# Kernel optimization log

Measured on AMD Instinct MI355X. Metric: run time of the kernel, lower is better.

## Reference

```python
import jax, jax.numpy as jnp
import numpy as np

DAMPENING = 0.3          # dampening_factor
REC_DAMPENING = 0.4      # recurrent_dampening_factor
DT = 1.0
MAX_DELAY = 5
N_BASIS = 5


@jax.custom_vjp
def spike_function(v_scaled):
    # hard threshold with triangular pseudo-derivative (custom gradient)
    return (v_scaled > 0.0).astype(v_scaled.dtype)

def _spike_fwd(v_scaled):
    return spike_function(v_scaled), v_scaled

def _spike_bwd(v_scaled, g):
    return (g * DAMPENING * jnp.maximum(1.0 - jnp.abs(v_scaled), 0.0),)

spike_function.defvjp(_spike_fwd, _spike_bwd)


def setup_inputs() -> dict:
    key = jax.random.key(0)
    ks = jax.random.split(key, 12)
    N, E, T, B = 50000, 2_000_000, 40, 1
    D, n5 = MAX_DELAY, N * N_BASIS
    inp = {}
    inp['weights'] = jax.random.normal(ks[0], (E,), jnp.float32) * 0.01
    inp['edge_basis'] = jax.random.uniform(ks[1], (E, N_BASIS), jnp.float32)
    inp['ext_input'] = jax.random.normal(ks[2], (B, T, n5), jnp.float32) * 0.02
    inp['decay'] = 0.9 + 0.09 * jax.random.uniform(ks[3], (N,), jnp.float32)
    inp['current_factor'] = jax.random.uniform(ks[4], (N,), jnp.float32)
    inp['gathered_g'] = jax.random.normal(ks[5], (N,), jnp.float32) * 0.01
    inp['v_th'] = jnp.ones((N,), jnp.float32)          # normalized threshold
    inp['v_reset'] = jnp.zeros((N,), jnp.float32)
    inp['normalizer'] = jnp.ones((N,), jnp.float32)    # v_th - e_l
    inp['t_ref'] = 2.0 * jnp.ones((N,), jnp.float32)
    inp['exp_dt_k'] = 0.8 + 0.19 * jax.random.uniform(ks[6], (N, 2), jnp.float32)
    inp['asc_amps'] = jax.random.normal(ks[7], (N, 2), jnp.float32) * 0.01
    inp['syn_decay'] = jax.random.uniform(ks[8], (n5,), jnp.float32)
    inp['psc_initial'] = jax.random.uniform(ks[9], (n5,), jnp.float32)
    inp['pre_idx'] = jax.random.randint(ks[10], (E,), 0, D * N, jnp.int32)
    inp['post_idx'] = jax.random.randint(ks[11], (E,), 0, N, jnp.int32)
    return inp


def reference(weights, edge_basis, ext_input, decay, current_factor, gathered_g,
              v_th, v_reset, normalizer, t_ref, exp_dt_k, asc_amps,
              syn_decay, psc_initial, pre_idx, post_idx):
    B, T, n5 = ext_input.shape
    N = n5 // N_BASIS
    D = MAX_DELAY
    # per-edge weight across the 5 synaptic basis filters: [E,5]
    ew = weights[:, None] * edge_basis

    def rec_input(z_flat):  # z_flat: [B, D*N] delayed spike buffer (flattened)
        zg = jnp.take(z_flat, pre_idx, axis=1)                # [B,E] gather presynaptic spikes
        contrib = zg[:, :, None] * ew[None]                    # [B,E,5]
        out = jax.vmap(lambda c: jax.ops.segment_sum(c, post_idx, num_segments=N))(contrib)
        return out.reshape(B, N * N_BASIS)                     # [B,N*5]

    def step(carry, x_t):
        v, r, asc, psc, z_buf = carry
        # recurrent dampening: scale gradient through recurrent spikes
        zd = z_buf * REC_DAMPENING
        zb = jax.lax.stop_gradient(z_buf - zd) + zd
        i_rec = rec_input(zb.reshape(B, D * N))
        new_psc = psc * syn_decay + (i_rec + x_t) * psc_initial      # [B,N*5]
        input_current = new_psc.reshape(B, N, N_BASIS).sum(-1)       # [B,N]
        prev_z = z_buf[:, 0]                                         # most recent spikes
        new_asc = exp_dt_k * asc + prev_z[:, :, None] * asc_amps     # [B,N,2]
        c1 = input_current + new_asc.sum(-1) + gathered_g
        new_v = decay * v + current_factor * c1
        new_v = jnp.where(prev_z > 0.5, v_reset, new_v)              # hard reset
        v_sc = (new_v - v_th) / normalizer
        z = spike_function(v_sc)
        z = jnp.where(r > 0.0, jnp.zeros_like(z), z)                 # refractory block
        new_r = jnp.maximum(r + z * t_ref - DT, 0.0)
        new_buf = jnp.concatenate([z[:, None], z_buf[:, :-1]], axis=1)
        return (new_v, new_r, new_asc, new_psc, new_buf), z

    v0 = jnp.broadcast_to(v_reset, (B, N)).astype(jnp.float32)
    r0 = jnp.zeros((B, N), jnp.float32)
    asc0 = jnp.zeros((B, N, 2), jnp.float32)
    psc0 = jnp.zeros((B, n5), jnp.float32)
    buf0 = jnp.zeros((B, D, N), jnp.float32)
    x_seq = jnp.transpose(ext_input, (1, 0, 2))  # [T,B,N*5]
    _, z_seq = jax.lax.scan(step, (v0, r0, asc0, psc0, buf0), x_seq)
    return jnp.transpose(z_seq, (1, 0, 2))  # [B,T,N] spikes
```

## Files before the change

### kernel.cpp

```cpp
#include <hip/hip_runtime.h>

#define NB_ 5
#define MD_ 5
#define CSL 128
#define CAP 6144
#define CH2 4096
#define RING 6


__global__ __launch_bounds__(256) void partition_kernel(
    const int* __restrict__ pre_idx,
    int* __restrict__ gcur,
    unsigned* __restrict__ part,
    int E, int N)
{
    __shared__ unsigned srt[CH2];
    __shared__ unsigned short bkt[CH2];
    __shared__ int hist[512];
    __shared__ int lbase[512];
    __shared__ int pos[512];
    __shared__ int gbase[512];
    __shared__ int tmp[256];

    const int t  = threadIdx.x;
    const int e0 = blockIdx.x * CH2;
    const int cnt = min(CH2, E - e0);

    hist[t] = 0; hist[t + 256] = 0;
    __syncthreads();

    for (int i = t; i < cnt; i += 256) {
        int pre = pre_idx[e0 + i];
        int d = pre / N;
        int n = pre - d * N;
        atomicAdd(&hist[n >> 7], 1);
    }
    __syncthreads();

    int a = hist[2 * t], b = hist[2 * t + 1], s = a + b;
    tmp[t] = s;
    __syncthreads();
    int x = s;
    for (int off = 1; off < 256; off <<= 1) {
        int y = (t >= off) ? tmp[t - off] : 0;
        __syncthreads();
        x += y;
        tmp[t] = x;
        __syncthreads();
    }
    int ep = x - s;
    lbase[2 * t] = ep;         pos[2 * t] = ep;
    lbase[2 * t + 1] = ep + a; pos[2 * t + 1] = ep + a;
    gbase[2 * t]     = a ? atomicAdd(&gcur[2 * t], a) : 0;
    gbase[2 * t + 1] = b ? atomicAdd(&gcur[2 * t + 1], b) : 0;
    __syncthreads();

    for (int i = t; i < cnt; i += 256) {
        int pre = pre_idx[e0 + i];
        int d = pre / N;
        int n = pre - d * N;
        int bk = n >> 7;
        int p = atomicAdd(&pos[bk], 1);
        srt[p] = ((unsigned)(n & (CSL - 1)) << 24) | ((unsigned)d << 21)
               | (unsigned)(e0 + i);
        bkt[p] = (unsigned short)bk;
    }
    __syncthreads();

    for (int j = t; j < cnt; j += 256) {
        int bk = bkt[j];
        int off2 = gbase[bk] + (j - lbase[bk]);
        if (off2 < CAP)
            part[(size_t)bk * CAP + off2] = srt[j];
    }
}

__global__ __launch_bounds__(256) void bucket_sort_kernel(
    const int* __restrict__ gcur,
    const unsigned* __restrict__ part,
    unsigned* __restrict__ edgeRec,
    uint2* __restrict__ rp,
    const float* __restrict__ decay, const float* __restrict__ cf,
    const float* __restrict__ g,     const float* __restrict__ vth,
    const float* __restrict__ vrst,  const float* __restrict__ nrm,
    const float* __restrict__ tref,  const float* __restrict__ ek,
    const float* __restrict__ am,
    float4* __restrict__ pk, float* __restrict__ v,
    int N)
{
    __shared__ int h[CSL];
    __shared__ int sc_[CSL];
    __shared__ int pos_[CSL];
    int c = blockIdx.x, t = threadIdx.x;

    if (t < CSL) {
        int n = c * CSL + t;
        if (n < N) {
            pk[3 * n]     = make_float4(decay[n], cf[n], g[n], vth[n]);
            pk[3 * n + 1] = make_float4(vrst[n], nrm[n], tref[n], ek[2 * n]);
            pk[3 * n + 2] = make_float4(ek[2 * n + 1], am[2 * n], am[2 * n + 1], 0.0f);
            v[n] = vrst[n];
        }
    }

    int cnt = min(gcur[c], CAP);
    size_t base = (size_t)c * CAP;
    if (t < CSL) h[t] = 0;
    __syncthreads();
    for (int i = t; i < cnt; i += 256)
        atomicAdd(&h[part[base + i] >> 24], 1);
    __syncthreads();
    if (t < CSL) sc_[t] = h[t];
    __syncthreads();
    for (int off = 1; off < CSL; off <<= 1) {
        int y = 0;
        if (t < CSL && t >= off) y = sc_[t - off];
        __syncthreads();
        if (t < CSL && t >= off) sc_[t] += y;
        __syncthreads();
    }
    if (t < CSL) {
        int end = sc_[t];
        pos_[t] = (int)base + end - h[t];
        int gn = c * CSL + t;
        if (gn < N)
            rp[gn] = make_uint2((unsigned)(base + end - h[t]),
                                (unsigned)(base + end));
    }
    __syncthreads();
    for (int i = t; i < cnt; i += 256) {
        unsigned q = part[base + i];
        int dst = atomicAdd(&pos_[q >> 24], 1);
        edgeRec[dst] = q;
    }
}


__global__ __launch_bounds__(256) void step_kernel(
    const float* __restrict__ x_t,
    float*       __restrict__ psc,
    const float* __restrict__ sd,
    const float* __restrict__ pi,
    const float4* __restrict__ pk,
    float* __restrict__ v,
    float* __restrict__ r,
    float* __restrict__ asc,
    float* __restrict__ ring,
    const int* __restrict__ scnt,
    int*       __restrict__ scnt_new,
    const float* __restrict__ out_prev,
    float*       __restrict__ out_t,
    const uint2*    __restrict__ rp,
    const unsigned* __restrict__ edgeRec,
    const float*    __restrict__ weights,
    const float*    __restrict__ edge_basis,
    const int*      __restrict__ post_idx,
    int t, int n5, int N)
{
    const int tloc = threadIdx.x;
    const int n = blockIdx.x * blockDim.x + tloc;
    const bool has = (n < N);
    const int lane = tloc & 63;

    const int* sw = scnt + t;
    int scw = sw[0] + sw[1] + sw[2] + sw[3] + sw[4];

    float z = 0.0f;
    if (has) {
        float ir0 = 0.f, ir1 = 0.f, ir2 = 0.f, ir3 = 0.f, ir4 = 0.f;
        float* rg = ring + (size_t)(t % RING) * n5 + (size_t)n * NB_;
        if (scw > 0) {
            ir0 = rg[0]; ir1 = rg[1]; ir2 = rg[2]; ir3 = rg[3]; ir4 = rg[4];
            rg[0] = 0.f; rg[1] = 0.f; rg[2] = 0.f; rg[3] = 0.f; rg[4] = 0.f;
        }

        const float* xp  = x_t + (size_t)n * NB_;
        float*       pp  = psc + (size_t)n * NB_;
        const float* sdp = sd  + (size_t)n * NB_;
        const float* pip = pi  + (size_t)n * NB_;
        float ic = 0.0f, pv;
        pv = pp[0] * sdp[0] + (ir0 + xp[0]) * pip[0]; pp[0] = pv; ic += pv;
        pv = pp[1] * sdp[1] + (ir1 + xp[1]) * pip[1]; pp[1] = pv; ic += pv;
        pv = pp[2] * sdp[2] + (ir2 + xp[2]) * pip[2]; pp[2] = pv; ic += pv;
        pv = pp[3] * sdp[3] + (ir3 + xp[3]) * pip[3]; pp[3] = pv; ic += pv;
        pv = pp[4] * sdp[4] + (ir4 + xp[4]) * pip[4]; pp[4] = pv; ic += pv;

        float4 P0 = pk[3 * n], P1 = pk[3 * n + 1], P2 = pk[3 * n + 2];

        float pz = (t > 0) ? out_prev[n] : 0.0f;

        float a0 = P1.w * asc[2 * n]     + pz * P2.y;
        float a1 = P2.x * asc[2 * n + 1] + pz * P2.z;
        asc[2 * n]     = a0;
        asc[2 * n + 1] = a1;

        float c1 = ic + (a0 + a1) + P0.z;
        float nv = P0.x * v[n] + P0.y * c1;
        if (pz > 0.5f) nv = P1.x;

        float vsc = (nv - P0.w) / P1.y;
        z = (vsc > 0.0f) ? 1.0f : 0.0f;
        float rr = r[n];
        if (rr > 0.0f) z = 0.0f;

        r[n] = fmaxf(rr + z * P1.z - 1.0f, 0.0f);
        v[n] = nv;
        out_t[n] = z;
    }

    unsigned long long fm = __ballot(z != 0.0f);
    if (lane == 0 && fm)
        atomicAdd(scnt_new, (int)__popcll(fm));

    if (fm) {
        unsigned rs0 = 0, re0 = 0;
        if (z != 0.0f) { uint2 row = rp[n]; rs0 = row.x; re0 = row.y; }

        unsigned long long fm2 = fm;
        while (fm2) {
            int src = (int)(__ffsll((long long)fm2) - 1);
            fm2 &= fm2 - 1;
            unsigned rs = __shfl(rs0, src);
            unsigned re = __shfl(re0, src);
            for (unsigned i = rs + lane; i < re; i += 64) {
                unsigned q = edgeRec[i];
                int d = (int)((q >> 21) & 7u);
                int e = (int)(q & 0x1FFFFFu);
                float w = weights[e];
                const float* bs = edge_basis + (size_t)e * NB_;
                float* dst = ring + (size_t)((t + 1 + d) % RING) * n5
                           + (size_t)post_idx[e] * NB_;
                atomicAdd(dst + 0, w * bs[0]);
                atomicAdd(dst + 1, w * bs[1]);
                atomicAdd(dst + 2, w * bs[2]);
                atomicAdd(dst + 3, w * bs[3]);
                atomicAdd(dst + 4, w * bs[4]);
            }
        }
    }
}


extern "C" void kernel_launch(void* const* d_in, const int* in_sizes, int n_in,
                              void* d_out, int out_size, void* d_ws, size_t ws_size,
                              hipStream_t stream)
{
    const float* weights        = (const float*)d_in[0];
    const float* edge_basis     = (const float*)d_in[1];
    const float* ext_input      = (const float*)d_in[2];
    const float* decay          = (const float*)d_in[3];
    const float* current_factor = (const float*)d_in[4];
    const float* gathered_g     = (const float*)d_in[5];
    const float* v_th           = (const float*)d_in[6];
    const float* v_reset        = (const float*)d_in[7];
    const float* normalizer     = (const float*)d_in[8];
    const float* t_ref          = (const float*)d_in[9];
    const float* exp_dt_k       = (const float*)d_in[10];
    const float* asc_amps       = (const float*)d_in[11];
    const float* syn_decay      = (const float*)d_in[12];
    const float* psc_initial    = (const float*)d_in[13];
    const int*   pre_idx        = (const int*)d_in[14];
    const int*   post_idx       = (const int*)d_in[15];

    const int E  = in_sizes[0];
    const int N  = in_sizes[3];
    const int n5 = N * NB_;
    const int T  = in_sizes[2] / n5;

    const int NC = (N + CSL - 1) / CSL;

    float* out = (float*)d_out;

    char* wsb = (char*)d_ws;
    size_t o = 0;
    int*   gcur = (int*)(wsb + o);   o += 512 * 4;
    int*   scnt = (int*)(wsb + o);   o += (size_t)(T + MD_) * 4;
    o = (o + 15) & ~(size_t)15;
    float* psc  = (float*)(wsb + o); o += (size_t)n5 * 4;
    float* r    = (float*)(wsb + o); o += (size_t)N * 4;
    float* asc  = (float*)(wsb + o); o += (size_t)2 * N * 4;
    o = (o + 15) & ~(size_t)15;
    float* ring = (float*)(wsb + o); o += (size_t)RING * n5 * 4;
    size_t zero_bytes = o;
    float*  v       = (float*)(wsb + o);  o += (size_t)N * 4;
    float4* pk      = (float4*)(wsb + o); o += (size_t)N * 12 * 4;
    uint2*  rp      = (uint2*)(wsb + o);  o += (size_t)N * 8;
    o = (o + 15) & ~(size_t)15;
    unsigned* part    = (unsigned*)(wsb + o); o += (size_t)NC * CAP * 4;
    unsigned* edgeRec = (unsigned*)(wsb + o); o += (size_t)NC * CAP * 4;

    hipMemsetAsync(d_ws, 0, zero_bytes, stream);

    const int nbe = (E + CH2 - 1) / CH2;
    partition_kernel<<<nbe, 256, 0, stream>>>(pre_idx, gcur, part, E, N);
    bucket_sort_kernel<<<NC, 256, 0, stream>>>(
        gcur, part, edgeRec, rp,
        decay, current_factor, gathered_g, v_th, v_reset, normalizer, t_ref,
        exp_dt_k, asc_amps, pk, v, N);

    const int nblk = (N + 255) / 256;
    for (int t = 0; t < T; ++t) {
        step_kernel<<<nblk, 256, 0, stream>>>(
            ext_input + (size_t)t * n5,
            psc, syn_decay, psc_initial,
            pk, v, r, asc,
            ring, scnt, scnt + MD_ + t,
            out + (size_t)(t > 0 ? t - 1 : 0) * N,
            out + (size_t)t * N,
            rp, edgeRec, weights, edge_basis, post_idx,
            t, n5, N);
    }
}
```

Before: 251.5 us.

## Pack per-neuron constants and state into float4 AoS records for step kernel

Per-neuron constants (synaptic decay, psc initial, neuron params, CSR row range) go into six contiguous float4s, and mutable state (psc, asc, v, r, previous spike) into three float4s per neuron. Each step now does wide vector loads and stores instead of many scattered scalar accesses across separate arrays, and no longer re-reads the previous output. This cuts memory transactions per step. The cost is a larger per-neuron stride, with some unused padding lanes being loaded.

```diff
diff --git a/kernel.cpp b/kernel.cpp
--- a/kernel.cpp
+++ b/kernel.cpp
@@ -79,13 +79,13 @@
     const int* __restrict__ gcur,
     const unsigned* __restrict__ part,
     unsigned* __restrict__ edgeRec,
-    uint2* __restrict__ rp,
     const float* __restrict__ decay, const float* __restrict__ cf,
     const float* __restrict__ g,     const float* __restrict__ vth,
     const float* __restrict__ vrst,  const float* __restrict__ nrm,
     const float* __restrict__ tref,  const float* __restrict__ ek,
     const float* __restrict__ am,
-    float4* __restrict__ pk, float* __restrict__ v,
+    const float* __restrict__ sd,    const float* __restrict__ pi,
+    float4* __restrict__ constC, float4* __restrict__ state,
     int N)
 {
     __shared__ int h[CSL];
@@ -93,16 +93,6 @@
     __shared__ int pos_[CSL];
     int c = blockIdx.x, t = threadIdx.x;
 
-    if (t < CSL) {
-        int n = c * CSL + t;
-        if (n < N) {
-            pk[3 * n]     = make_float4(decay[n], cf[n], g[n], vth[n]);
-            pk[3 * n + 1] = make_float4(vrst[n], nrm[n], tref[n], ek[2 * n]);
-            pk[3 * n + 2] = make_float4(ek[2 * n + 1], am[2 * n], am[2 * n + 1], 0.0f);
-            v[n] = vrst[n];
-        }
-    }
-
     int cnt = min(gcur[c], CAP);
     size_t base = (size_t)c * CAP;
     if (t < CSL) h[t] = 0;
@@ -122,10 +112,24 @@
     if (t < CSL) {
         int end = sc_[t];
         pos_[t] = (int)base + end - h[t];
-        int gn = c * CSL + t;
-        if (gn < N)
-            rp[gn] = make_uint2((unsigned)(base + end - h[t]),
-                                (unsigned)(base + end));
+        int n = c * CSL + t;
+        if (n < N) {
+            unsigned rs = (unsigned)(base + end - h[t]);
+            unsigned re = (unsigned)(base + end);
+            const float* sdp = sd + (size_t)n * NB_;
+            const float* pip = pi + (size_t)n * NB_;
+            constC[6 * (size_t)n + 0] = make_float4(sdp[0], sdp[1], sdp[2], sdp[3]);
+            constC[6 * (size_t)n + 1] = make_float4(sdp[4], pip[0], pip[1], pip[2]);
+            constC[6 * (size_t)n + 2] = make_float4(pip[3], pip[4], decay[n], cf[n]);
+            constC[6 * (size_t)n + 3] = make_float4(g[n], vth[n], vrst[n], nrm[n]);
+            constC[6 * (size_t)n + 4] = make_float4(tref[n], ek[2 * n], ek[2 * n + 1], am[2 * n]);
+            constC[6 * (size_t)n + 5] = make_float4(am[2 * n + 1],
+                                                    __uint_as_float(rs),
+                                                    __uint_as_float(re), 0.0f);
+            state[3 * (size_t)n + 0] = make_float4(0.f, 0.f, 0.f, 0.f);
+            state[3 * (size_t)n + 1] = make_float4(0.f, 0.f, 0.f, vrst[n]);
+            state[3 * (size_t)n + 2] = make_float4(0.f, 0.f, 0.f, 0.f);
+        }
     }
     __syncthreads();
     for (int i = t; i < cnt; i += 256) {
@@ -138,19 +142,12 @@
 
 __global__ __launch_bounds__(256) void step_kernel(
     const float* __restrict__ x_t,
-    float*       __restrict__ psc,
-    const float* __restrict__ sd,
-    const float* __restrict__ pi,
-    const float4* __restrict__ pk,
-    float* __restrict__ v,
-    float* __restrict__ r,
-    float* __restrict__ asc,
+    const float4* __restrict__ constC,
+    float4*       __restrict__ state,
     float* __restrict__ ring,
     const int* __restrict__ scnt,
     int*       __restrict__ scnt_new,
-    const float* __restrict__ out_prev,
     float*       __restrict__ out_t,
-    const uint2*    __restrict__ rp,
     const unsigned* __restrict__ edgeRec,
     const float*    __restrict__ weights,
     const float*    __restrict__ edge_basis,
@@ -166,7 +163,17 @@
     int scw = sw[0] + sw[1] + sw[2] + sw[3] + sw[4];
 
     float z = 0.0f;
+    unsigned rs0 = 0, re0 = 0;
     if (has) {
+        float4 C0 = constC[6 * (size_t)n + 0];
+        float4 C1 = constC[6 * (size_t)n + 1];
+        float4 C2 = constC[6 * (size_t)n + 2];
+        float4 C3 = constC[6 * (size_t)n + 3];
+        float4 C4 = constC[6 * (size_t)n + 4];
+        float4 S0 = state[3 * (size_t)n + 0];
+        float4 S1 = state[3 * (size_t)n + 1];
+        float4 S2 = state[3 * (size_t)n + 2];
+
         float ir0 = 0.f, ir1 = 0.f, ir2 = 0.f, ir3 = 0.f, ir4 = 0.f;
         float* rg = ring + (size_t)(t % RING) * n5 + (size_t)n * NB_;
         if (scw > 0) {
@@ -174,38 +181,40 @@
             rg[0] = 0.f; rg[1] = 0.f; rg[2] = 0.f; rg[3] = 0.f; rg[4] = 0.f;
         }
 
-        const float* xp  = x_t + (size_t)n * NB_;
-        float*       pp  = psc + (size_t)n * NB_;
-        const float* sdp = sd  + (size_t)n * NB_;
-        const float* pip = pi  + (size_t)n * NB_;
+        const float* xp = x_t + (size_t)n * NB_;
         float ic = 0.0f, pv;
-        pv = pp[0] * sdp[0] + (ir0 + xp[0]) * pip[0]; pp[0] = pv; ic += pv;
-        pv = pp[1] * sdp[1] + (ir1 + xp[1]) * pip[1]; pp[1] = pv; ic += pv;
-        pv = pp[2] * sdp[2] + (ir2 + xp[2]) * pip[2]; pp[2] = pv; ic += pv;
-        pv = pp[3] * sdp[3] + (ir3 + xp[3]) * pip[3]; pp[3] = pv; ic += pv;
-        pv = pp[4] * sdp[4] + (ir4 + xp[4]) * pip[4]; pp[4] = pv; ic += pv;
-
-        float4 P0 = pk[3 * n], P1 = pk[3 * n + 1], P2 = pk[3 * n + 2];
-
-        float pz = (t > 0) ? out_prev[n] : 0.0f;
-
-        float a0 = P1.w * asc[2 * n]     + pz * P2.y;
-        float a1 = P2.x * asc[2 * n + 1] + pz * P2.z;
-        asc[2 * n]     = a0;
-        asc[2 * n + 1] = a1;
-
-        float c1 = ic + (a0 + a1) + P0.z;
-        float nv = P0.x * v[n] + P0.y * c1;
-        if (pz > 0.5f) nv = P1.x;
-
-        float vsc = (nv - P0.w) / P1.y;
+        float p0, p1, p2, p3, p4;
+        pv = S0.x * C0.x + (ir0 + xp[0]) * C1.y; p0 = pv; ic += pv;
+        pv = S0.y * C0.y + (ir1 + xp[1]) * C1.z; p1 = pv; ic += pv;
+        pv = S0.z * C0.z + (ir2 + xp[2]) * C1.w; p2 = pv; ic += pv;
+        pv = S0.w * C0.w + (ir3 + xp[3]) * C2.x; p3 = pv; ic += pv;
+        pv = S1.x * C1.x + (ir4 + xp[4]) * C2.y; p4 = pv; ic += pv;
+
+        float pz = S2.y;
+
+        float a0 = C4.y * S1.y + pz * C4.w;
+        float a1 = C4.z * S1.z + pz * ((float4&)constC[6 * (size_t)n + 5]).x;
+        float4 C5 = constC[6 * (size_t)n + 5];
+        a1 = C4.z * S1.z + pz * C5.x;
+
+        float c1 = ic + (a0 + a1) + C3.x;
+        float nv = C2.z * S1.w + C2.w * c1;
+        if (pz > 0.5f) nv = C3.z;
+
+        float vsc = (nv - C3.y) / C3.w;
         z = (vsc > 0.0f) ? 1.0f : 0.0f;
-        float rr = r[n];
+        float rr = S2.x;
         if (rr > 0.0f) z = 0.0f;
 
-        r[n] = fmaxf(rr + z * P1.z - 1.0f, 0.0f);
-        v[n] = nv;
+        float nr = fmaxf(rr + z * C4.x - 1.0f, 0.0f);
+
+        state[3 * (size_t)n + 0] = make_float4(p0, p1, p2, p3);
+        state[3 * (size_t)n + 1] = make_float4(p4, a0, a1, nv);
+        state[3 * (size_t)n + 2] = make_float4(nr, z, 0.0f, 0.0f);
         out_t[n] = z;
+
+        rs0 = __float_as_uint(C5.y);
+        re0 = __float_as_uint(C5.z);
     }
 
     unsigned long long fm = __ballot(z != 0.0f);
@@ -213,9 +222,6 @@
         atomicAdd(scnt_new, (int)__popcll(fm));
 
     if (fm) {
-        unsigned rs0 = 0, re0 = 0;
-        if (z != 0.0f) { uint2 row = rp[n]; rs0 = row.x; re0 = row.y; }
-
         unsigned long long fm2 = fm;
         while (fm2) {
             int src = (int)(__ffsll((long long)fm2) - 1);
@@ -276,16 +282,10 @@
     int*   gcur = (int*)(wsb + o);   o += 512 * 4;
     int*   scnt = (int*)(wsb + o);   o += (size_t)(T + MD_) * 4;
     o = (o + 15) & ~(size_t)15;
-    float* psc  = (float*)(wsb + o); o += (size_t)n5 * 4;
-    float* r    = (float*)(wsb + o); o += (size_t)N * 4;
-    float* asc  = (float*)(wsb + o); o += (size_t)2 * N * 4;
-    o = (o + 15) & ~(size_t)15;
     float* ring = (float*)(wsb + o); o += (size_t)RING * n5 * 4;
     size_t zero_bytes = o;
-    float*  v       = (float*)(wsb + o);  o += (size_t)N * 4;
-    float4* pk      = (float4*)(wsb + o); o += (size_t)N * 12 * 4;
-    uint2*  rp      = (uint2*)(wsb + o);  o += (size_t)N * 8;
-    o = (o + 15) & ~(size_t)15;
+    float4* constC = (float4*)(wsb + o); o += (size_t)N * 6 * 16;
+    float4* state  = (float4*)(wsb + o); o += (size_t)N * 3 * 16;
     unsigned* part    = (unsigned*)(wsb + o); o += (size_t)NC * CAP * 4;
     unsigned* edgeRec = (unsigned*)(wsb + o); o += (size_t)NC * CAP * 4;
 
@@ -294,20 +294,19 @@
     const int nbe = (E + CH2 - 1) / CH2;
     partition_kernel<<<nbe, 256, 0, stream>>>(pre_idx, gcur, part, E, N);
     bucket_sort_kernel<<<NC, 256, 0, stream>>>(
-        gcur, part, edgeRec, rp,
+        gcur, part, edgeRec,
         decay, current_factor, gathered_g, v_th, v_reset, normalizer, t_ref,
-        exp_dt_k, asc_amps, pk, v, N);
+        exp_dt_k, asc_amps, syn_decay, psc_initial,
+        constC, state, N);
 
     const int nblk = (N + 255) / 256;
     for (int t = 0; t < T; ++t) {
         step_kernel<<<nblk, 256, 0, stream>>>(
             ext_input + (size_t)t * n5,
-            psc, syn_decay, psc_initial,
-            pk, v, r, asc,
+            constC, state,
             ring, scnt, scnt + MD_ + t,
-            out + (size_t)(t > 0 ? t - 1 : 0) * N,
             out + (size_t)t * N,
-            rp, edgeRec, weights, edge_basis, post_idx,
+            edgeRec, weights, edge_basis, post_idx,
             t, n5, N);
     }
 }
```

After: 235.4 us. 1.07x faster.
